# Optimization experiments

Measured on AMD Instinct MI355X. Metric: run time of the kernel, lower is better.

The kernel has to match this reference:

```python
import jax, jax.numpy as jnp
import numpy as np

N_NODES = 100000
N_EDGES = 3200000
IN_CH = 32
HID = 64


def gcn_conv(x, src, dst, W, b, n_nodes):
    """PyG GCNConv with default add_self_loops=True and symmetric normalization.
    out = D^{-1/2} (A + I) D^{-1/2} X W + b, where D is degree of A+I."""
    h = x @ W  # [N, out]
    ones = jnp.ones((src.shape[0],), dtype=h.dtype)
    deg = jax.ops.segment_sum(ones, dst, num_segments=n_nodes) + 1.0  # +1 self loop
    dinv = jax.lax.rsqrt(deg)  # [N]
    norm = dinv[src] * dinv[dst]  # [E]
    msgs = h[src] * norm[:, None]  # [E, out] gather (memory-bound)
    agg = jax.ops.segment_sum(msgs, dst, num_segments=n_nodes)  # scatter-add
    agg = agg + h * (1.0 / deg)[:, None]  # self-loop contribution (norm = 1/deg)
    return agg + b


def setup_inputs() -> dict:
    key = jax.random.key(0)
    ks = jax.random.split(key, 8)
    x = jax.random.normal(ks[0], (N_NODES, IN_CH), dtype=jnp.float32)
    edge_index = jax.random.randint(ks[1], (2, N_EDGES), 0, N_NODES, dtype=jnp.int64)
    # Glorot-style init for GCN weights, uniform for linear layer
    s1 = (6.0 / (IN_CH + HID)) ** 0.5
    s2 = (6.0 / (HID + HID)) ** 0.5
    W1 = jax.random.uniform(ks[2], (IN_CH, HID), jnp.float32, -s1, s1)
    b1 = jnp.zeros((HID,), jnp.float32)
    W2 = jax.random.uniform(ks[3], (HID, HID), jnp.float32, -s2, s2)
    b2 = jnp.zeros((HID,), jnp.float32)
    sc = 1.0 / (HID ** 0.5)
    Wc = jax.random.uniform(ks[4], (HID, 1), jnp.float32, -sc, sc)
    bc = jax.random.uniform(ks[5], (1,), jnp.float32, -sc, sc)
    return {"x": x, "edge_index": edge_index, "W1": W1, "b1": b1,
            "W2": W2, "b2": b2, "Wc": Wc, "bc": bc}


def reference(x, edge_index, W1, b1, W2, b2, Wc, bc):
    src, dst = edge_index[0], edge_index[1]
    n = x.shape[0]
    h = jax.nn.relu(gcn_conv(x, src, dst, W1, b1, n))
    h = jax.nn.relu(gcn_conv(h, src, dst, W2, b2, n))
    return jax.nn.sigmoid(h @ Wc + bc)  # [N, 1]
```

## Files before the change

kernel.cpp:

```cpp
#include <hip/hip_runtime.h>
#include <math.h>

#define N_NODES 100000
#define N_EDGES 3200000
#define IN_CH 32
#define HID 64
#define BW 512
#define NB ((N_NODES + BW - 1) / BW)
#define CAP 17408
#define K3_CHUNK 8192
#define K3_BLOCKS ((N_EDGES + K3_CHUNK - 1) / K3_CHUNK)

typedef unsigned short ushort_t;
typedef unsigned long long u64_t;

__device__ __forceinline__ float bflo(unsigned u) { return __uint_as_float(u << 16); }
__device__ __forceinline__ float bfhi(unsigned u) { return __uint_as_float(u & 0xffff0000u); }
__device__ __forceinline__ unsigned packbf(float a, float b) {
    unsigned ua = __float_as_uint(a); ua += 0x7fffu + ((ua >> 16) & 1u);
    unsigned ub = __float_as_uint(b); ub += 0x7fffu + ((ub >> 16) & 1u);
    return (ua >> 16) | (ub & 0xffff0000u);
}

__global__ void partition_kernel(const int* __restrict__ src, const int* __restrict__ dst,
                                 int* __restrict__ gcursor, int* __restrict__ gsw) {
    __shared__ int h[NB], lbase[NB], lcur[NB];
    int t = threadIdx.x;
    for (int i = t; i < NB; i += 256) { h[i] = 0; lcur[i] = 0; }
    __syncthreads();
    const int4* d4 = (const int4*)dst;
    const int4* s4 = (const int4*)src;
    int i0 = blockIdx.x * (K3_CHUNK / 4) + t;
#pragma unroll
    for (int j = 0; j < K3_CHUNK / 1024; ++j) {
        int i4 = i0 + j * 256;
        if (i4 < N_EDGES / 4) {
            int4 d = d4[i4];
            atomicAdd(&h[d.x >> 9], 1);
            atomicAdd(&h[d.y >> 9], 1);
            atomicAdd(&h[d.z >> 9], 1);
            atomicAdd(&h[d.w >> 9], 1);
        }
    }
    __syncthreads();
    for (int i = t; i < NB; i += 256)
        lbase[i] = h[i] ? atomicAdd(&gcursor[i], h[i]) : 0;
    __syncthreads();
#pragma unroll
    for (int j = 0; j < K3_CHUNK / 1024; ++j) {
        int i4 = i0 + j * 256;
        if (i4 < N_EDGES / 4) {
            int4 d = d4[i4];
            int4 s = s4[i4];
            int b, r, idx;
            b = d.x >> 9; r = atomicAdd(&lcur[b], 1); idx = lbase[b] + r;
            if (idx < CAP) gsw[(size_t)b * CAP + idx] = s.x | ((d.x & (BW - 1)) << 17);
            b = d.y >> 9; r = atomicAdd(&lcur[b], 1); idx = lbase[b] + r;
            if (idx < CAP) gsw[(size_t)b * CAP + idx] = s.y | ((d.y & (BW - 1)) << 17);
            b = d.z >> 9; r = atomicAdd(&lcur[b], 1); idx = lbase[b] + r;
            if (idx < CAP) gsw[(size_t)b * CAP + idx] = s.z | ((d.z & (BW - 1)) << 17);
            b = d.w >> 9; r = atomicAdd(&lcur[b], 1); idx = lbase[b] + r;
            if (idx < CAP) gsw[(size_t)b * CAP + idx] = s.w | ((d.w & (BW - 1)) << 17);
        }
    }
}

__global__ void scan_buckets_kernel(const int* __restrict__ gcursor, int* __restrict__ gbase,
                                    int* __restrict__ rowptr) {
    __shared__ int sa[256], sb[256];
    int t = threadIdx.x;
    int v = (t < NB) ? gcursor[t] : 0;
    sa[t] = v;
    __syncthreads();
    int* pa = sa; int* pb = sb;
    for (int off = 1; off < 256; off <<= 1) {
        int add = (t >= off) ? pa[t - off] : 0;
        pb[t] = pa[t] + add;
        __syncthreads();
        int* tmp = pa; pa = pb; pb = tmp;
    }
    int excl = pa[t] - v;
    if (t <= NB) gbase[t] = (t == NB) ? N_EDGES : excl;
    if (t == 0) rowptr[N_NODES] = N_EDGES;
}

__global__ __launch_bounds__(512) void bucket_place_kernel(
        const int* __restrict__ gsw, const int* __restrict__ gcursor,
        const int* __restrict__ gbase,
        int* __restrict__ rowptr, float* __restrict__ dinv, int* __restrict__ esw) {
    __shared__ int cnt[BW], exc[BW], cur[BW];
    __shared__ int sa[BW], sb[BW];
    int t = threadIdx.x;
    int k = blockIdx.x;
    int d0 = k * BW;
    cnt[t] = 0; cur[t] = 0;
    __syncthreads();
    int total = gcursor[k];
    if (total > CAP) total = CAP;
    const int* reg = gsw + (size_t)k * CAP;
    for (int i = t; i < total; i += 512)
        atomicAdd(&cnt[reg[i] >> 17], 1);
    __syncthreads();
    sa[t] = cnt[t];
    __syncthreads();
    int* pa = sa; int* pb = sb;
    for (int off = 1; off < BW; off <<= 1) {
        int add = (t >= off) ? pa[t - off] : 0;
        pb[t] = pa[t] + add;
        __syncthreads();
        int* tmp = pa; pa = pb; pb = tmp;
    }
    int e_x = pa[t] - cnt[t];
    exc[t] = e_x;
    int cbase = gbase[k];
    int d = d0 + t;
    if (d < N_NODES) {
        rowptr[d] = cbase + e_x;
        dinv[d] = rsqrtf((float)cnt[t] + 1.0f);
    }
    __syncthreads();
    for (int i = t; i < total; i += 512) {
        int u = reg[i];
        int ld = u >> 17;
        int r = atomicAdd(&cur[ld], 1);
        esw[cbase + exc[ld] + r] = u & 0x1FFFF;
    }
}

__global__ void xs_kernel(const float* __restrict__ X, const float* __restrict__ dinv,
                          ushort_t* __restrict__ Xs) {
    int i = blockIdx.x * blockDim.x + threadIdx.x;
    if (i >= N_NODES * 8) return;
    int node = i >> 3;
    float di = dinv[node];
    const float4* X4 = (const float4*)X;
    float4 v = X4[i];
    u64_t o = ((u64_t)packbf(v.z * di, v.w * di) << 32) | packbf(v.x * di, v.y * di);
    *(u64_t*)((uint2*)Xs + i) = o;
}

__global__ void gather_x_kernel(const int* __restrict__ esw, const int* __restrict__ rowptr,
                                const float* __restrict__ dinv, const ushort_t* __restrict__ Xs,
                                float* __restrict__ y) {
    int t = threadIdx.x;
    int node = blockIdx.x * 4 + (t >> 6);
    int lane = t & 63;
    int g = lane >> 3, s = lane & 7;
    int beg = rowptr[node], end = rowptr[node + 1];
    const uint2* H8 = (const uint2*)Xs;
    float4 acc = make_float4(0.f, 0.f, 0.f, 0.f);
    int i = beg + g;
    for (; i + 8 < end; i += 16) {
        int s0 = esw[i];
        int s1 = esw[i + 8];
        uint2 v0 = H8[(size_t)s0 * 8 + s];
        uint2 v1 = H8[(size_t)s1 * 8 + s];
        acc.x += bflo(v0.x) + bflo(v1.x);
        acc.y += bfhi(v0.x) + bfhi(v1.x);
        acc.z += bflo(v0.y) + bflo(v1.y);
        acc.w += bfhi(v0.y) + bfhi(v1.y);
    }
    if (i < end) {
        int s0 = esw[i];
        uint2 v0 = H8[(size_t)s0 * 8 + s];
        acc.x += bflo(v0.x);
        acc.y += bfhi(v0.x);
        acc.z += bflo(v0.y);
        acc.w += bfhi(v0.y);
    }
    acc.x += __shfl_xor(acc.x, 8, 64);  acc.y += __shfl_xor(acc.y, 8, 64);
    acc.z += __shfl_xor(acc.z, 8, 64);  acc.w += __shfl_xor(acc.w, 8, 64);
    acc.x += __shfl_xor(acc.x, 16, 64); acc.y += __shfl_xor(acc.y, 16, 64);
    acc.z += __shfl_xor(acc.z, 16, 64); acc.w += __shfl_xor(acc.w, 16, 64);
    acc.x += __shfl_xor(acc.x, 32, 64); acc.y += __shfl_xor(acc.y, 32, 64);
    acc.z += __shfl_xor(acc.z, 32, 64); acc.w += __shfl_xor(acc.w, 32, 64);

    if (g == 0) {
        uint2 hn = H8[(size_t)node * 8 + s];
        float di = dinv[node];
        float4 r;
        r.x = di * (acc.x + bflo(hn.x));
        r.y = di * (acc.y + bfhi(hn.x));
        r.z = di * (acc.z + bflo(hn.y));
        r.w = di * (acc.w + bfhi(hn.y));
        ((float4*)y)[(size_t)node * 8 + s] = r;
    }
}

__global__ void dense12_kernel(const float* __restrict__ y, const float* __restrict__ W1,
                               const float* __restrict__ b1, const float* __restrict__ W2,
                               const float* __restrict__ dinv, ushort_t* __restrict__ Hs2) {
    __shared__ float W1l[IN_CH * HID];
    __shared__ float W2l[HID * HID];
    __shared__ float Yl[16 * IN_CH];
    __shared__ float H1l[16 * HID];
    int t = threadIdx.x;
    int node0 = blockIdx.x * 16;
    for (int i = t; i < IN_CH * HID; i += 256) W1l[i] = W1[i];
    for (int i = t; i < HID * HID; i += 256) W2l[i] = W2[i];
    for (int i = t; i < 16 * IN_CH; i += 256) Yl[i] = y[(size_t)node0 * IN_CH + i];
    __syncthreads();
    int nl = t >> 4;
    int c16 = t & 15;
    float4 bb = ((const float4*)b1)[c16];
    float s0 = bb.x, s1 = bb.y, s2 = bb.z, s3 = bb.w;
    const float4* W14 = (const float4*)W1l;
#pragma unroll
    for (int k = 0; k < IN_CH; ++k) {
        float xv = Yl[nl * IN_CH + k];
        float4 w = W14[k * 16 + c16];
        s0 += xv * w.x; s1 += xv * w.y; s2 += xv * w.z; s3 += xv * w.w;
    }
    H1l[nl * HID + c16 * 4 + 0] = fmaxf(s0, 0.f);
    H1l[nl * HID + c16 * 4 + 1] = fmaxf(s1, 0.f);
    H1l[nl * HID + c16 * 4 + 2] = fmaxf(s2, 0.f);
    H1l[nl * HID + c16 * 4 + 3] = fmaxf(s3, 0.f);
    __syncthreads();
    float r0 = 0.f, r1 = 0.f, r2 = 0.f, r3 = 0.f;
    const float4* W24 = (const float4*)W2l;
#pragma unroll
    for (int k = 0; k < HID; ++k) {
        float hv = H1l[nl * HID + k];
        float4 w = W24[k * 16 + c16];
        r0 += hv * w.x; r1 += hv * w.y; r2 += hv * w.z; r3 += hv * w.w;
    }
    int node = node0 + nl;
    float di = dinv[node];
    u64_t o = ((u64_t)packbf(r2 * di, r3 * di) << 32) | packbf(r0 * di, r1 * di);
    *(u64_t*)(Hs2 + (size_t)node * HID + c16 * 4) = o;
}

__global__ void gather_cls_kernel(const int* __restrict__ esw, const int* __restrict__ rowptr,
                                  const float* __restrict__ dinv, const ushort_t* __restrict__ Hs,
                                  const float* __restrict__ b,
                                  const float* __restrict__ Wc, const float* __restrict__ bc,
                                  float* __restrict__ out) {
    int t = threadIdx.x;
    int node = blockIdx.x * 4 + (t >> 6);
    int lane = t & 63;
    int g = lane >> 4, s = lane & 15;
    int beg = rowptr[node], end = rowptr[node + 1];
    int cnt = end - beg;
    const uint2* H8 = (const uint2*)Hs;
    float4 acc = make_float4(0.f, 0.f, 0.f, 0.f);
    int i = g;
    for (; i + 12 < cnt; i += 16) {
        int s0 = esw[beg + i];
        int s1 = esw[beg + i + 4];
        int s2 = esw[beg + i + 8];
        int s3 = esw[beg + i + 12];
        uint2 v0 = H8[(size_t)s0 * 16 + s];
        uint2 v1 = H8[(size_t)s1 * 16 + s];
        uint2 v2 = H8[(size_t)s2 * 16 + s];
        uint2 v3 = H8[(size_t)s3 * 16 + s];
        acc.x += (bflo(v0.x) + bflo(v1.x)) + (bflo(v2.x) + bflo(v3.x));
        acc.y += (bfhi(v0.x) + bfhi(v1.x)) + (bfhi(v2.x) + bfhi(v3.x));
        acc.z += (bflo(v0.y) + bflo(v1.y)) + (bflo(v2.y) + bflo(v3.y));
        acc.w += (bfhi(v0.y) + bfhi(v1.y)) + (bfhi(v2.y) + bfhi(v3.y));
    }
    for (; i < cnt; i += 4) {
        int s0 = esw[beg + i];
        uint2 v0 = H8[(size_t)s0 * 16 + s];
        acc.x += bflo(v0.x);
        acc.y += bfhi(v0.x);
        acc.z += bflo(v0.y);
        acc.w += bfhi(v0.y);
    }
    acc.x += __shfl_xor(acc.x, 16, 64); acc.y += __shfl_xor(acc.y, 16, 64);
    acc.z += __shfl_xor(acc.z, 16, 64); acc.w += __shfl_xor(acc.w, 16, 64);
    acc.x += __shfl_xor(acc.x, 32, 64); acc.y += __shfl_xor(acc.y, 32, 64);
    acc.z += __shfl_xor(acc.z, 32, 64); acc.w += __shfl_xor(acc.w, 32, 64);

    uint2 hn = H8[(size_t)node * 16 + s];
    float di = dinv[node];
    float4 bb = ((const float4*)b)[s];
    float rx = fmaxf(di * (acc.x + bflo(hn.x)) + bb.x, 0.f);
    float ry = fmaxf(di * (acc.y + bfhi(hn.x)) + bb.y, 0.f);
    float rz = fmaxf(di * (acc.z + bflo(hn.y)) + bb.z, 0.f);
    float rw = fmaxf(di * (acc.w + bfhi(hn.y)) + bb.w, 0.f);

    float4 wc = ((const float4*)Wc)[s];
    float v = rx * wc.x + ry * wc.y + rz * wc.z + rw * wc.w;
#pragma unroll
    for (int off = 1; off < 16; off <<= 1) v += __shfl_xor(v, off, 64);
    if (lane == 0) out[node] = 1.0f / (1.0f + expf(-(v + bc[0])));
}

extern "C" void kernel_launch(void* const* d_in, const int* in_sizes, int n_in,
                              void* d_out, int out_size, void* d_ws, size_t ws_size,
                              hipStream_t stream) {
    const float* x  = (const float*)d_in[0];
    const int* ei   = (const int*)d_in[1];
    const float* W1 = (const float*)d_in[2];
    const float* b1 = (const float*)d_in[3];
    const float* W2 = (const float*)d_in[4];
    const float* b2 = (const float*)d_in[5];
    const float* Wc = (const float*)d_in[6];
    const float* bc = (const float*)d_in[7];
    float* out = (float*)d_out;

    const int* src = ei;
    const int* dst = ei + N_EDGES;

    int*   gsw    = (int*)d_ws;
    int*   esw    = gsw + (size_t)NB * CAP;
    int*   rowptr = esw + N_EDGES;
    float* dinv   = (float*)(rowptr + N_NODES + 8);
    int*   gcursor= (int*)(dinv + N_NODES);
    int*   gbase  = gcursor + 512;
    ushort_t* Xs  = (ushort_t*)(gbase + 512);
    float*    y   = (float*)(Xs + (size_t)N_NODES * IN_CH);
    ushort_t* Hs2 = (ushort_t*)(y + (size_t)N_NODES * IN_CH);

    int node16 = N_NODES / 16;
    int node4  = N_NODES / 4;

    hipMemsetAsync(gcursor, 0, NB * sizeof(int), stream);
    partition_kernel<<<K3_BLOCKS, 256, 0, stream>>>(src, dst, gcursor, gsw);
    scan_buckets_kernel<<<1, 256, 0, stream>>>(gcursor, gbase, rowptr);
    bucket_place_kernel<<<NB, 512, 0, stream>>>(gsw, gcursor, gbase, rowptr, dinv, esw);

    xs_kernel<<<(N_NODES * 8 + 255) / 256, 256, 0, stream>>>(x, dinv, Xs);
    gather_x_kernel<<<node4, 256, 0, stream>>>(esw, rowptr, dinv, Xs, y);
    dense12_kernel<<<node16, 256, 0, stream>>>(y, W1, b1, W2, dinv, Hs2);

    gather_cls_kernel<<<node4, 256, 0, stream>>>(esw, rowptr, dinv, Hs2, b2, Wc, bc, out);
}
```

Baseline: 249.8 us.

## Fuse X scaling into bucket placement, store y as bf16, widen dense tile

```diff
diff --git a/kernel.cpp b/kernel.cpp
--- a/kernel.cpp
+++ b/kernel.cpp
@@ -8,7 +8,7 @@
 #define BW 512
 #define NB ((N_NODES + BW - 1) / BW)
 #define CAP 17408
-#define K3_CHUNK 8192
+#define K3_CHUNK 4096
 #define K3_BLOCKS ((N_EDGES + K3_CHUNK - 1) / K3_CHUNK)
 
 typedef unsigned short ushort_t;
@@ -84,64 +84,67 @@
     if (t == 0) rowptr[N_NODES] = N_EDGES;
 }
 
-__global__ __launch_bounds__(512) void bucket_place_kernel(
+__global__ __launch_bounds__(1024) void bucket_place_kernel(
         const int* __restrict__ gsw, const int* __restrict__ gcursor,
-        const int* __restrict__ gbase,
-        int* __restrict__ rowptr, float* __restrict__ dinv, int* __restrict__ esw) {
+        const int* __restrict__ gbase, const float* __restrict__ X,
+        int* __restrict__ rowptr, float* __restrict__ dinv, int* __restrict__ esw,
+        ushort_t* __restrict__ Xs) {
     __shared__ int cnt[BW], exc[BW], cur[BW];
     __shared__ int sa[BW], sb[BW];
     int t = threadIdx.x;
     int k = blockIdx.x;
     int d0 = k * BW;
-    cnt[t] = 0; cur[t] = 0;
+    if (t < BW) { cnt[t] = 0; cur[t] = 0; }
     __syncthreads();
     int total = gcursor[k];
     if (total > CAP) total = CAP;
     const int* reg = gsw + (size_t)k * CAP;
-    for (int i = t; i < total; i += 512)
+    for (int i = t; i < total; i += 1024)
         atomicAdd(&cnt[reg[i] >> 17], 1);
     __syncthreads();
-    sa[t] = cnt[t];
+    if (t < BW) sa[t] = cnt[t];
     __syncthreads();
     int* pa = sa; int* pb = sb;
     for (int off = 1; off < BW; off <<= 1) {
-        int add = (t >= off) ? pa[t - off] : 0;
-        pb[t] = pa[t] + add;
+        if (t < BW) {
+            int add = (t >= off) ? pa[t - off] : 0;
+            pb[t] = pa[t] + add;
+        }
         __syncthreads();
         int* tmp = pa; pa = pb; pb = tmp;
     }
-    int e_x = pa[t] - cnt[t];
-    exc[t] = e_x;
     int cbase = gbase[k];
-    int d = d0 + t;
-    if (d < N_NODES) {
-        rowptr[d] = cbase + e_x;
-        dinv[d] = rsqrtf((float)cnt[t] + 1.0f);
-    }
-    __syncthreads();
-    for (int i = t; i < total; i += 512) {
+    if (t < BW) {
+        int e_x = pa[t] - cnt[t];
+        exc[t] = e_x;
+        int d = d0 + t;
+        if (d < N_NODES) {
+            rowptr[d] = cbase + e_x;
+            dinv[d] = rsqrtf((float)cnt[t] + 1.0f);
+        }
+    }
+    __syncthreads();
+    for (int i = t; i < total; i += 1024) {
         int u = reg[i];
         int ld = u >> 17;
         int r = atomicAdd(&cur[ld], 1);
         esw[cbase + exc[ld] + r] = u & 0x1FFFF;
     }
-}
-
-__global__ void xs_kernel(const float* __restrict__ X, const float* __restrict__ dinv,
-                          ushort_t* __restrict__ Xs) {
-    int i = blockIdx.x * blockDim.x + threadIdx.x;
-    if (i >= N_NODES * 8) return;
-    int node = i >> 3;
-    float di = dinv[node];
     const float4* X4 = (const float4*)X;
-    float4 v = X4[i];
-    u64_t o = ((u64_t)packbf(v.z * di, v.w * di) << 32) | packbf(v.x * di, v.y * di);
-    *(u64_t*)((uint2*)Xs + i) = o;
+    for (int i = t; i < BW * 8; i += 1024) {
+        int nl = i >> 3;
+        int node = d0 + nl;
+        if (node >= N_NODES) break;
+        float di = rsqrtf((float)cnt[nl] + 1.0f);
+        float4 v = X4[(size_t)node * 8 + (i & 7)];
+        u64_t o = ((u64_t)packbf(v.z * di, v.w * di) << 32) | packbf(v.x * di, v.y * di);
+        *(u64_t*)((uint2*)Xs + (size_t)node * 8 + (i & 7)) = o;
+    }
 }
 
 __global__ void gather_x_kernel(const int* __restrict__ esw, const int* __restrict__ rowptr,
                                 const float* __restrict__ dinv, const ushort_t* __restrict__ Xs,
-                                float* __restrict__ y) {
+                                ushort_t* __restrict__ y) {
     int t = threadIdx.x;
     int node = blockIdx.x * 4 + (t >> 6);
     int lane = t & 63;
@@ -178,56 +181,75 @@
     if (g == 0) {
         uint2 hn = H8[(size_t)node * 8 + s];
         float di = dinv[node];
-        float4 r;
-        r.x = di * (acc.x + bflo(hn.x));
-        r.y = di * (acc.y + bfhi(hn.x));
-        r.z = di * (acc.z + bflo(hn.y));
-        r.w = di * (acc.w + bfhi(hn.y));
-        ((float4*)y)[(size_t)node * 8 + s] = r;
-    }
-}
-
-__global__ void dense12_kernel(const float* __restrict__ y, const float* __restrict__ W1,
-                               const float* __restrict__ b1, const float* __restrict__ W2,
-                               const float* __restrict__ dinv, ushort_t* __restrict__ Hs2) {
+        float rx = di * (acc.x + bflo(hn.x));
+        float ry = di * (acc.y + bfhi(hn.x));
+        float rz = di * (acc.z + bflo(hn.y));
+        float rw = di * (acc.w + bfhi(hn.y));
+        u64_t o = ((u64_t)packbf(rz, rw) << 32) | packbf(rx, ry);
+        *(u64_t*)((uint2*)y + (size_t)node * 8 + s) = o;
+    }
+}
+
+__global__ __launch_bounds__(256) void dense12_kernel(
+        const ushort_t* __restrict__ ybf, const float* __restrict__ W1,
+        const float* __restrict__ b1, const float* __restrict__ W2,
+        const float* __restrict__ dinv, ushort_t* __restrict__ Hs2) {
     __shared__ float W1l[IN_CH * HID];
     __shared__ float W2l[HID * HID];
-    __shared__ float Yl[16 * IN_CH];
-    __shared__ float H1l[16 * HID];
-    int t = threadIdx.x;
-    int node0 = blockIdx.x * 16;
-    for (int i = t; i < IN_CH * HID; i += 256) W1l[i] = W1[i];
-    for (int i = t; i < HID * HID; i += 256) W2l[i] = W2[i];
-    for (int i = t; i < 16 * IN_CH; i += 256) Yl[i] = y[(size_t)node0 * IN_CH + i];
-    __syncthreads();
-    int nl = t >> 4;
-    int c16 = t & 15;
-    float4 bb = ((const float4*)b1)[c16];
-    float s0 = bb.x, s1 = bb.y, s2 = bb.z, s3 = bb.w;
-    const float4* W14 = (const float4*)W1l;
+    __shared__ float Yl[32 * IN_CH];
+    __shared__ float H1l[32 * HID];
+    int t = threadIdx.x;
+    int node0 = blockIdx.x * 32;
+    for (int i = t; i < IN_CH * HID / 4; i += 256) ((float4*)W1l)[i] = ((const float4*)W1)[i];
+    for (int i = t; i < HID * HID / 4; i += 256) ((float4*)W2l)[i] = ((const float4*)W2)[i];
+    {
+        uint2 v = ((const uint2*)ybf)[(size_t)node0 * 8 + t];
+        int nl = t >> 3, ci = t & 7;
+        Yl[nl * IN_CH + ci * 4 + 0] = bflo(v.x);
+        Yl[nl * IN_CH + ci * 4 + 1] = bfhi(v.x);
+        Yl[nl * IN_CH + ci * 4 + 2] = bflo(v.y);
+        Yl[nl * IN_CH + ci * 4 + 3] = bfhi(v.y);
+    }
+    __syncthreads();
+    int nl = t >> 3;
+    int c8 = t & 7;
+    int ch0 = c8 * 8;
+    float4 bA = ((const float4*)b1)[c8 * 2];
+    float4 bB = ((const float4*)b1)[c8 * 2 + 1];
+    float a0 = bA.x, a1 = bA.y, a2 = bA.z, a3 = bA.w;
+    float a4 = bB.x, a5 = bB.y, a6 = bB.z, a7 = bB.w;
 #pragma unroll
     for (int k = 0; k < IN_CH; ++k) {
         float xv = Yl[nl * IN_CH + k];
-        float4 w = W14[k * 16 + c16];
-        s0 += xv * w.x; s1 += xv * w.y; s2 += xv * w.z; s3 += xv * w.w;
-    }
-    H1l[nl * HID + c16 * 4 + 0] = fmaxf(s0, 0.f);
-    H1l[nl * HID + c16 * 4 + 1] = fmaxf(s1, 0.f);
-    H1l[nl * HID + c16 * 4 + 2] = fmaxf(s2, 0.f);
-    H1l[nl * HID + c16 * 4 + 3] = fmaxf(s3, 0.f);
+        float4 wA = *(const float4*)&W1l[k * HID + ch0];
+        float4 wB = *(const float4*)&W1l[k * HID + ch0 + 4];
+        a0 += xv * wA.x; a1 += xv * wA.y; a2 += xv * wA.z; a3 += xv * wA.w;
+        a4 += xv * wB.x; a5 += xv * wB.y; a6 += xv * wB.z; a7 += xv * wB.w;
+    }
+    float* hp = &H1l[nl * HID + ch0];
+    hp[0] = fmaxf(a0, 0.f); hp[1] = fmaxf(a1, 0.f);
+    hp[2] = fmaxf(a2, 0.f); hp[3] = fmaxf(a3, 0.f);
+    hp[4] = fmaxf(a4, 0.f); hp[5] = fmaxf(a5, 0.f);
+    hp[6] = fmaxf(a6, 0.f); hp[7] = fmaxf(a7, 0.f);
     __syncthreads();
     float r0 = 0.f, r1 = 0.f, r2 = 0.f, r3 = 0.f;
-    const float4* W24 = (const float4*)W2l;
+    float r4 = 0.f, r5 = 0.f, r6 = 0.f, r7 = 0.f;
 #pragma unroll
     for (int k = 0; k < HID; ++k) {
         float hv = H1l[nl * HID + k];
-        float4 w = W24[k * 16 + c16];
-        r0 += hv * w.x; r1 += hv * w.y; r2 += hv * w.z; r3 += hv * w.w;
+        float4 wA = *(const float4*)&W2l[k * HID + ch0];
+        float4 wB = *(const float4*)&W2l[k * HID + ch0 + 4];
+        r0 += hv * wA.x; r1 += hv * wA.y; r2 += hv * wA.z; r3 += hv * wA.w;
+        r4 += hv * wB.x; r5 += hv * wB.y; r6 += hv * wB.z; r7 += hv * wB.w;
     }
     int node = node0 + nl;
     float di = dinv[node];
-    u64_t o = ((u64_t)packbf(r2 * di, r3 * di) << 32) | packbf(r0 * di, r1 * di);
-    *(u64_t*)(Hs2 + (size_t)node * HID + c16 * 4) = o;
+    uint4 o;
+    o.x = packbf(r0 * di, r1 * di);
+    o.y = packbf(r2 * di, r3 * di);
+    o.z = packbf(r4 * di, r5 * di);
+    o.w = packbf(r6 * di, r7 * di);
+    *(uint4*)(Hs2 + (size_t)node * HID + ch0) = o;
 }
 
 __global__ void gather_cls_kernel(const int* __restrict__ esw, const int* __restrict__ rowptr,
@@ -309,20 +331,20 @@
     int*   gcursor= (int*)(dinv + N_NODES);
     int*   gbase  = gcursor + 512;
     ushort_t* Xs  = (ushort_t*)(gbase + 512);
-    float*    y   = (float*)(Xs + (size_t)N_NODES * IN_CH);
-    ushort_t* Hs2 = (ushort_t*)(y + (size_t)N_NODES * IN_CH);
-
-    int node16 = N_NODES / 16;
+    ushort_t* y   = Xs + (size_t)N_NODES * IN_CH;
+    ushort_t* Hs2 = y + (size_t)N_NODES * IN_CH;
+
+    int node32 = N_NODES / 32;
     int node4  = N_NODES / 4;
 
     hipMemsetAsync(gcursor, 0, NB * sizeof(int), stream);
     partition_kernel<<<K3_BLOCKS, 256, 0, stream>>>(src, dst, gcursor, gsw);
     scan_buckets_kernel<<<1, 256, 0, stream>>>(gcursor, gbase, rowptr);
-    bucket_place_kernel<<<NB, 512, 0, stream>>>(gsw, gcursor, gbase, rowptr, dinv, esw);
-
-    xs_kernel<<<(N_NODES * 8 + 255) / 256, 256, 0, stream>>>(x, dinv, Xs);
+    bucket_place_kernel<<<NB, 1024, 0, stream>>>(gsw, gcursor, gbase, x,
+                                                 rowptr, dinv, esw, Xs);
+
     gather_x_kernel<<<node4, 256, 0, stream>>>(esw, rowptr, dinv, Xs, y);
-    dense12_kernel<<<node16, 256, 0, stream>>>(y, W1, b1, W2, dinv, Hs2);
+    dense12_kernel<<<node32, 256, 0, stream>>>(y, W1, b1, W2, dinv, Hs2);
 
     gather_cls_kernel<<<node4, 256, 0, stream>>>(esw, rowptr, dinv, Hs2, b2, Wc, bc, out);
 }
```

New measurement: 252.3 us. No clear change (+1.0%).
